# Kernel optimization log

Measured on AMD Instinct MI355X. Metric: run time of the kernel, lower is better.

The kernel has to match this reference:

```python
import jax, jax.numpy as jnp
import numpy as np

IN_F = 1024
OUT_F = 1024

def setup_inputs() -> dict:
    key = jax.random.key(0)
    ks = jax.random.split(key, 7)
    s = 1.0 / np.sqrt(IN_F)
    x = jax.random.normal(ks[0], (4, 2048, IN_F), dtype=jnp.float32)
    Wq = jax.random.uniform(ks[1], (OUT_F, IN_F), jnp.float32, -s, s)
    bq = jax.random.uniform(ks[2], (OUT_F,), jnp.float32, -s, s)
    Wk = jax.random.uniform(ks[3], (OUT_F, IN_F), jnp.float32, -s, s)
    bk = jax.random.uniform(ks[4], (OUT_F,), jnp.float32, -s, s)
    Wv = jax.random.uniform(ks[5], (OUT_F, IN_F), jnp.float32, -s, s)
    bv = jax.random.uniform(ks[6], (OUT_F,), jnp.float32, -s, s)
    return {"x": x, "Wq": Wq, "bq": bq, "Wk": Wk, "bk": bk, "Wv": Wv, "bv": bv}

def reference(x, Wq, bq, Wk, bk, Wv, bv):
    # Projector: ReLU(Linear(x))
    q = jax.nn.relu(jnp.einsum('bsd,od->bso', x, Wq) + bq)  # [B,S,O]
    k = jax.nn.relu(jnp.einsum('bsd,od->bso', x, Wk) + bk)
    v = jax.nn.relu(jnp.einsum('bsd,od->bso', x, Wv) + bv)
    logits = jnp.einsum('bio,bko->bik', q, k)  # unscaled QK^T, [B,S,S]
    scores = jax.nn.softmax(logits, axis=-1)
    out = jnp.einsum('bik,bko->bio', scores, v)
    return out
```

## Files before the change

### kernel.cpp

```cpp
#include <hip/hip_runtime.h>
#include <hip/hip_bf16.h>


#define SEQ 2048
#define DIM 1024
#define NB 4
#define MTOT (NB * SEQ)

typedef __attribute__((ext_vector_type(8))) short frag_ab;
typedef __attribute__((ext_vector_type(4))) float frag_cd;

__device__ __forceinline__ ushort f2bf(float f) {
    union { float f; unsigned u; } x; x.f = f;
    unsigned r = x.u + 0x7fffu + ((x.u >> 16) & 1u);
    return (ushort)(r >> 16);
}

__global__ __launch_bounds__(256) void qkv_kernel(
    const float* __restrict__ x,
    const float* __restrict__ Wq, const float* __restrict__ bq,
    const float* __restrict__ Wk, const float* __restrict__ bk,
    const float* __restrict__ Wv, const float* __restrict__ bv,
    ushort* __restrict__ q, ushort* __restrict__ k, ushort* __restrict__ v)
{
    const float* W; const float* bias; ushort* out;
    if (blockIdx.z == 0)      { W = Wq; bias = bq; out = q; }
    else if (blockIdx.z == 1) { W = Wk; bias = bk; out = k; }
    else                      { W = Wv; bias = bv; out = v; }

    __shared__ ushort As[128][40];
    __shared__ ushort Bs[128][40];

    const int tid  = threadIdx.x;
    const int wave = tid >> 6;
    const int lane = tid & 63;
    const int l16  = lane & 15;
    const int quad = lane >> 4;
    const int m0 = blockIdx.x * 128;
    const int n0 = blockIdx.y * 128;
    const int wm = (wave & 1) * 64;
    const int wn = (wave >> 1) * 64;

    const int sr = tid >> 3;
    const int sc = (tid & 7) * 4;

    frag_cd acc[4][4] = {};

    for (int k0 = 0; k0 < DIM; k0 += 32) {
        #pragma unroll
        for (int i = 0; i < 4; ++i) {
            int row = i * 32 + sr;
            float4 f = *(const float4*)&x[(size_t)(m0 + row) * DIM + k0 + sc];
            ushort4 u; u.x = f2bf(f.x); u.y = f2bf(f.y); u.z = f2bf(f.z); u.w = f2bf(f.w);
            *(ushort4*)&As[row][sc] = u;
        }
        #pragma unroll
        for (int i = 0; i < 4; ++i) {
            int row = i * 32 + sr;
            float4 f = *(const float4*)&W[(size_t)(n0 + row) * DIM + k0 + sc];
            ushort4 u; u.x = f2bf(f.x); u.y = f2bf(f.y); u.z = f2bf(f.z); u.w = f2bf(f.w);
            *(ushort4*)&Bs[row][sc] = u;
        }
        __syncthreads();
        frag_ab af[4], bfr[4];
        #pragma unroll
        for (int mi = 0; mi < 4; ++mi)
            af[mi] = *(const frag_ab*)&As[wm + mi * 16 + l16][quad * 8];
        #pragma unroll
        for (int ni = 0; ni < 4; ++ni)
            bfr[ni] = *(const frag_ab*)&Bs[wn + ni * 16 + l16][quad * 8];
        #pragma unroll
        for (int mi = 0; mi < 4; ++mi)
            #pragma unroll
            for (int ni = 0; ni < 4; ++ni)
                acc[mi][ni] = __builtin_amdgcn_mfma_f32_16x16x32_bf16(
                    af[mi], bfr[ni], acc[mi][ni], 0, 0, 0);
        __syncthreads();
    }

    #pragma unroll
    for (int ni = 0; ni < 4; ++ni) {
        int col = n0 + wn + ni * 16 + l16;
        float bb = bias[col];
        #pragma unroll
        for (int mi = 0; mi < 4; ++mi) {
            int rowb = m0 + wm + mi * 16 + quad * 4;
            #pragma unroll
            for (int r = 0; r < 4; ++r) {
                float val = acc[mi][ni][r] + bb;
                val = val > 0.0f ? val : 0.0f;
                out[(size_t)(rowb + r) * DIM + col] = f2bf(val);
            }
        }
    }
}

__global__ __launch_bounds__(256) void transpose_v(
    const ushort* __restrict__ v, ushort* __restrict__ vt)
{
    __shared__ ushort T[64][72];
    const int bz = blockIdx.z;
    const int s0 = blockIdx.x * 64;
    const int o0 = blockIdx.y * 64;
    const int t  = threadIdx.x;

    #pragma unroll
    for (int p = 0; p < 4; ++p) {
        int sl = p * 16 + (t >> 4);
        int o4 = (t & 15) * 4;
        ushort4 u = *(const ushort4*)&v[(size_t)(bz * SEQ + s0 + sl) * DIM + o0 + o4];
        *(ushort4*)&T[sl][o4] = u;
    }
    __syncthreads();
    #pragma unroll
    for (int p = 0; p < 4; ++p) {
        int ol = p * 16 + (t >> 4);
        int s4 = (t & 15) * 4;
        ushort4 u;
        u.x = T[s4 + 0][ol]; u.y = T[s4 + 1][ol];
        u.z = T[s4 + 2][ol]; u.w = T[s4 + 3][ol];
        *(ushort4*)&vt[(size_t)(bz * DIM + o0 + ol) * SEQ + s0 + s4] = u;
    }
}

__global__ __launch_bounds__(256) void qk_kernel(
    const ushort* __restrict__ q, const ushort* __restrict__ kk,
    float* __restrict__ logits)
{
    __shared__ ushort As[128][40];
    __shared__ ushort Bs[128][40];

    const int tid  = threadIdx.x;
    const int wave = tid >> 6;
    const int lane = tid & 63;
    const int l16  = lane & 15;
    const int quad = lane >> 4;
    const int bz = blockIdx.z;
    const int m0 = blockIdx.x * 128;
    const int n0 = blockIdx.y * 128;
    const int wm = (wave & 1) * 64;
    const int wn = (wave >> 1) * 64;
    const size_t base = (size_t)bz * SEQ;

    const int sr = tid >> 2;
    const int sc = (tid & 3) * 8;

    frag_cd acc[4][4] = {};

    for (int k0 = 0; k0 < DIM; k0 += 32) {
        #pragma unroll
        for (int i = 0; i < 2; ++i) {
            int row = i * 64 + sr;
            *(uint4*)&As[row][sc] =
                *(const uint4*)&q[(base + m0 + row) * DIM + k0 + sc];
            *(uint4*)&Bs[row][sc] =
                *(const uint4*)&kk[(base + n0 + row) * DIM + k0 + sc];
        }
        __syncthreads();
        frag_ab af[4], bfr[4];
        #pragma unroll
        for (int mi = 0; mi < 4; ++mi)
            af[mi] = *(const frag_ab*)&As[wm + mi * 16 + l16][quad * 8];
        #pragma unroll
        for (int ni = 0; ni < 4; ++ni)
            bfr[ni] = *(const frag_ab*)&Bs[wn + ni * 16 + l16][quad * 8];
        #pragma unroll
        for (int mi = 0; mi < 4; ++mi)
            #pragma unroll
            for (int ni = 0; ni < 4; ++ni)
                acc[mi][ni] = __builtin_amdgcn_mfma_f32_16x16x32_bf16(
                    af[mi], bfr[ni], acc[mi][ni], 0, 0, 0);
        __syncthreads();
    }

    #pragma unroll
    for (int mi = 0; mi < 4; ++mi) {
        int rowb = m0 + wm + mi * 16 + quad * 4;
        #pragma unroll
        for (int r = 0; r < 4; ++r) {
            #pragma unroll
            for (int ni = 0; ni < 4; ++ni) {
                int col = n0 + wn + ni * 16 + l16;
                logits[(base + rowb + r) * SEQ + col] = acc[mi][ni][r];
            }
        }
    }
}

__global__ __launch_bounds__(256) void softmax_kernel(float* __restrict__ logits)
{
    float* p = logits + (size_t)blockIdx.x * SEQ;
    const int t = threadIdx.x;
    const int wave = t >> 6, lane = t & 63;

    float4 a = ((const float4*)p)[t];
    float4 b = ((const float4*)p)[t + 256];

    float m = fmaxf(fmaxf(fmaxf(a.x, a.y), fmaxf(a.z, a.w)),
                    fmaxf(fmaxf(b.x, b.y), fmaxf(b.z, b.w)));
    #pragma unroll
    for (int off = 32; off; off >>= 1) m = fmaxf(m, __shfl_down(m, off, 64));

    __shared__ float red[4];
    if (lane == 0) red[wave] = m;
    __syncthreads();
    m = fmaxf(fmaxf(red[0], red[1]), fmaxf(red[2], red[3]));

    a.x = __expf(a.x - m); a.y = __expf(a.y - m);
    a.z = __expf(a.z - m); a.w = __expf(a.w - m);
    b.x = __expf(b.x - m); b.y = __expf(b.y - m);
    b.z = __expf(b.z - m); b.w = __expf(b.w - m);

    float s = (a.x + a.y + a.z + a.w) + (b.x + b.y + b.z + b.w);
    #pragma unroll
    for (int off = 32; off; off >>= 1) s += __shfl_down(s, off, 64);
    __syncthreads();
    if (lane == 0) red[wave] = s;
    __syncthreads();
    s = red[0] + red[1] + red[2] + red[3];
    float inv = 1.0f / s;

    ushort* o = (ushort*)p;
    ushort4 u0, u1;
    u0.x = f2bf(a.x * inv); u0.y = f2bf(a.y * inv);
    u0.z = f2bf(a.z * inv); u0.w = f2bf(a.w * inv);
    u1.x = f2bf(b.x * inv); u1.y = f2bf(b.y * inv);
    u1.z = f2bf(b.z * inv); u1.w = f2bf(b.w * inv);
    ((ushort4*)o)[t]       = u0;
    ((ushort4*)o)[t + 256] = u1;
}

__global__ __launch_bounds__(256) void pv_kernel(
    const ushort* __restrict__ probs, const ushort* __restrict__ vt,
    float* __restrict__ out)
{
    __shared__ ushort As[128][40];
    __shared__ ushort Bs[128][40];

    const int tid  = threadIdx.x;
    const int wave = tid >> 6;
    const int lane = tid & 63;
    const int l16  = lane & 15;
    const int quad = lane >> 4;
    const int bz = blockIdx.z;
    const int m0 = blockIdx.x * 128;
    const int n0 = blockIdx.y * 128;
    const int wm = (wave & 1) * 64;
    const int wn = (wave >> 1) * 64;

    const int sr = tid >> 2;
    const int sc = (tid & 3) * 8;

    frag_cd acc[4][4] = {};

    for (int k0 = 0; k0 < SEQ; k0 += 32) {
        #pragma unroll
        for (int i = 0; i < 2; ++i) {
            int row = i * 64 + sr;
            *(uint4*)&As[row][sc] =
                *(const uint4*)&probs[((size_t)(bz * SEQ + m0 + row)) * 4096 + k0 + sc];
            *(uint4*)&Bs[row][sc] =
                *(const uint4*)&vt[((size_t)(bz * DIM + n0 + row)) * SEQ + k0 + sc];
        }
        __syncthreads();
        frag_ab af[4], bfr[4];
        #pragma unroll
        for (int mi = 0; mi < 4; ++mi)
            af[mi] = *(const frag_ab*)&As[wm + mi * 16 + l16][quad * 8];
        #pragma unroll
        for (int ni = 0; ni < 4; ++ni)
            bfr[ni] = *(const frag_ab*)&Bs[wn + ni * 16 + l16][quad * 8];
        #pragma unroll
        for (int mi = 0; mi < 4; ++mi)
            #pragma unroll
            for (int ni = 0; ni < 4; ++ni)
                acc[mi][ni] = __builtin_amdgcn_mfma_f32_16x16x32_bf16(
                    af[mi], bfr[ni], acc[mi][ni], 0, 0, 0);
        __syncthreads();
    }

    #pragma unroll
    for (int mi = 0; mi < 4; ++mi) {
        int rowb = m0 + wm + mi * 16 + quad * 4;
        #pragma unroll
        for (int r = 0; r < 4; ++r) {
            #pragma unroll
            for (int ni = 0; ni < 4; ++ni) {
                int col = n0 + wn + ni * 16 + l16;
                out[((size_t)(bz * SEQ + rowb + r)) * DIM + col] = acc[mi][ni][r];
            }
        }
    }
}

extern "C" void kernel_launch(void* const* d_in, const int* in_sizes, int n_in,
                              void* d_out, int out_size, void* d_ws, size_t ws_size,
                              hipStream_t stream)
{
    const float* x  = (const float*)d_in[0];
    const float* Wq = (const float*)d_in[1];
    const float* bq = (const float*)d_in[2];
    const float* Wk = (const float*)d_in[3];
    const float* bk = (const float*)d_in[4];
    const float* Wv = (const float*)d_in[5];
    const float* bv = (const float*)d_in[6];
    float* out = (float*)d_out;

    ushort* q  = (ushort*)d_ws;
    ushort* kk = q  + (size_t)MTOT * DIM;
    ushort* v  = kk + (size_t)MTOT * DIM;
    ushort* vt = v  + (size_t)MTOT * DIM;
    float* logits = (float*)(vt + (size_t)MTOT * DIM);

    qkv_kernel<<<dim3(MTOT / 128, DIM / 128, 3), 256, 0, stream>>>(
        x, Wq, bq, Wk, bk, Wv, bv, q, kk, v);
    transpose_v<<<dim3(SEQ / 64, DIM / 64, NB), 256, 0, stream>>>(v, vt);
    qk_kernel<<<dim3(SEQ / 128, SEQ / 128, NB), 256, 0, stream>>>(q, kk, logits);
    softmax_kernel<<<NB * SEQ, 256, 0, stream>>>(logits);
    pv_kernel<<<dim3(SEQ / 128, DIM / 128, NB), 256, 0, stream>>>(
        (const ushort*)logits, vt, out);
}
```

Baseline: 321.9 us.

## Pre-convert inputs to bf16 and load GEMM tiles directly to LDS with swizzle

Adds separate kernels that convert x and the three weight matrices to bf16 once, so the QKV GEMM no longer re-converts fp32 tiles inside its inner loop. All three GEMMs now share a helper that uses global_load_lds to copy 16-byte chunks straight into an unpadded, XOR-swizzled LDS layout, which avoids register staging and bank conflicts. The cost is two extra launches and an extra pass over x through bf16 workspace buffers, with xb aliased over the logits region.

```diff
diff --git a/kernel.cpp b/kernel.cpp
--- a/kernel.cpp
+++ b/kernel.cpp
@@ -16,20 +16,97 @@
     return (ushort)(r >> 16);
 }
 
+typedef __attribute__((address_space(1))) const unsigned int guint;
+typedef __attribute__((address_space(3))) unsigned int luint;
+
+__device__ __forceinline__ void gld_lds16(const void* g, void* l) {
+    __builtin_amdgcn_global_load_lds((guint*)g, (luint*)l, 16, 0, 0);
+}
+
+__device__ __forceinline__ void gemm_tiles(
+    const ushort* __restrict__ A, size_t lda,
+    const ushort* __restrict__ B, size_t ldb, int K,
+    ushort* As, ushort* Bs, frag_cd (&acc)[4][4])
+{
+    const int tid  = threadIdx.x;
+    const int wave = tid >> 6;
+    const int lane = tid & 63;
+    const int l16  = lane & 15;
+    const int quad = lane >> 4;
+    const int sr = wave * 16 + (lane >> 2);
+    const int sc = lane & 3;
+
+    for (int k0 = 0; k0 < K; k0 += 32) {
+        #pragma unroll
+        for (int j = 0; j < 2; ++j) {
+            int row = j * 64 + sr;
+            int cg  = sc ^ ((row >> 1) & 3);
+            ushort* la = As + (j * 64 + wave * 16) * 32;
+            ushort* lb = Bs + (j * 64 + wave * 16) * 32;
+            gld_lds16(A + (size_t)row * lda + k0 + cg * 8, la);
+            gld_lds16(B + (size_t)row * ldb + k0 + cg * 8, lb);
+        }
+        __syncthreads();
+        frag_ab af[4], bfr[4];
+        const int wm = (wave & 1) * 64;
+        const int wn = (wave >> 1) * 64;
+        #pragma unroll
+        for (int mi = 0; mi < 4; ++mi) {
+            int row = wm + mi * 16 + l16;
+            int s = quad ^ ((row >> 1) & 3);
+            af[mi] = *(const frag_ab*)&As[row * 32 + s * 8];
+        }
+        #pragma unroll
+        for (int ni = 0; ni < 4; ++ni) {
+            int row = wn + ni * 16 + l16;
+            int s = quad ^ ((row >> 1) & 3);
+            bfr[ni] = *(const frag_ab*)&Bs[row * 32 + s * 8];
+        }
+        #pragma unroll
+        for (int mi = 0; mi < 4; ++mi)
+            #pragma unroll
+            for (int ni = 0; ni < 4; ++ni)
+                acc[mi][ni] = __builtin_amdgcn_mfma_f32_16x16x32_bf16(
+                    af[mi], bfr[ni], acc[mi][ni], 0, 0, 0);
+        __syncthreads();
+    }
+}
+
+__global__ __launch_bounds__(256) void cvt_x_kernel(
+    const float* __restrict__ src, ushort* __restrict__ dst)
+{
+    size_t i = (size_t)blockIdx.x * 256 + threadIdx.x;
+    float4 f = ((const float4*)src)[i];
+    ushort4 u; u.x = f2bf(f.x); u.y = f2bf(f.y); u.z = f2bf(f.z); u.w = f2bf(f.w);
+    ((ushort4*)dst)[i] = u;
+}
+
+__global__ __launch_bounds__(256) void cvt_w_kernel(
+    const float* __restrict__ Wq, const float* __restrict__ Wk,
+    const float* __restrict__ Wv, ushort* __restrict__ dst)
+{
+    const float* src = blockIdx.y == 0 ? Wq : (blockIdx.y == 1 ? Wk : Wv);
+    ushort* d = dst + (size_t)blockIdx.y * DIM * DIM;
+    size_t i = (size_t)blockIdx.x * 256 + threadIdx.x;
+    float4 f = ((const float4*)src)[i];
+    ushort4 u; u.x = f2bf(f.x); u.y = f2bf(f.y); u.z = f2bf(f.z); u.w = f2bf(f.w);
+    ((ushort4*)d)[i] = u;
+}
+
 __global__ __launch_bounds__(256) void qkv_kernel(
-    const float* __restrict__ x,
-    const float* __restrict__ Wq, const float* __restrict__ bq,
-    const float* __restrict__ Wk, const float* __restrict__ bk,
-    const float* __restrict__ Wv, const float* __restrict__ bv,
+    const ushort* __restrict__ xb, const ushort* __restrict__ Wb,
+    const float* __restrict__ bq, const float* __restrict__ bk,
+    const float* __restrict__ bv,
     ushort* __restrict__ q, ushort* __restrict__ k, ushort* __restrict__ v)
 {
-    const float* W; const float* bias; ushort* out;
-    if (blockIdx.z == 0)      { W = Wq; bias = bq; out = q; }
-    else if (blockIdx.z == 1) { W = Wk; bias = bk; out = k; }
-    else                      { W = Wv; bias = bv; out = v; }
-
-    __shared__ ushort As[128][40];
-    __shared__ ushort Bs[128][40];
+    const float* bias; ushort* out;
+    if (blockIdx.z == 0)      { bias = bq; out = q; }
+    else if (blockIdx.z == 1) { bias = bk; out = k; }
+    else                      { bias = bv; out = v; }
+    const ushort* W = Wb + (size_t)blockIdx.z * DIM * DIM;
+
+    __shared__ ushort As[128 * 32];
+    __shared__ ushort Bs[128 * 32];
 
     const int tid  = threadIdx.x;
     const int wave = tid >> 6;
@@ -41,42 +118,9 @@
     const int wm = (wave & 1) * 64;
     const int wn = (wave >> 1) * 64;
 
-    const int sr = tid >> 3;
-    const int sc = (tid & 7) * 4;
-
     frag_cd acc[4][4] = {};
-
-    for (int k0 = 0; k0 < DIM; k0 += 32) {
-        #pragma unroll
-        for (int i = 0; i < 4; ++i) {
-            int row = i * 32 + sr;
-            float4 f = *(const float4*)&x[(size_t)(m0 + row) * DIM + k0 + sc];
-            ushort4 u; u.x = f2bf(f.x); u.y = f2bf(f.y); u.z = f2bf(f.z); u.w = f2bf(f.w);
-            *(ushort4*)&As[row][sc] = u;
-        }
-        #pragma unroll
-        for (int i = 0; i < 4; ++i) {
-            int row = i * 32 + sr;
-            float4 f = *(const float4*)&W[(size_t)(n0 + row) * DIM + k0 + sc];
-            ushort4 u; u.x = f2bf(f.x); u.y = f2bf(f.y); u.z = f2bf(f.z); u.w = f2bf(f.w);
-            *(ushort4*)&Bs[row][sc] = u;
-        }
-        __syncthreads();
-        frag_ab af[4], bfr[4];
-        #pragma unroll
-        for (int mi = 0; mi < 4; ++mi)
-            af[mi] = *(const frag_ab*)&As[wm + mi * 16 + l16][quad * 8];
-        #pragma unroll
-        for (int ni = 0; ni < 4; ++ni)
-            bfr[ni] = *(const frag_ab*)&Bs[wn + ni * 16 + l16][quad * 8];
-        #pragma unroll
-        for (int mi = 0; mi < 4; ++mi)
-            #pragma unroll
-            for (int ni = 0; ni < 4; ++ni)
-                acc[mi][ni] = __builtin_amdgcn_mfma_f32_16x16x32_bf16(
-                    af[mi], bfr[ni], acc[mi][ni], 0, 0, 0);
-        __syncthreads();
-    }
+    gemm_tiles(xb + (size_t)m0 * DIM, DIM, W + (size_t)n0 * DIM, DIM, DIM,
+               As, Bs, acc);
 
     #pragma unroll
     for (int ni = 0; ni < 4; ++ni) {
@@ -127,8 +171,8 @@
     const ushort* __restrict__ q, const ushort* __restrict__ kk,
     float* __restrict__ logits)
 {
-    __shared__ ushort As[128][40];
-    __shared__ ushort Bs[128][40];
+    __shared__ ushort As[128 * 32];
+    __shared__ ushort Bs[128 * 32];
 
     const int tid  = threadIdx.x;
     const int wave = tid >> 6;
@@ -142,48 +186,20 @@
     const int wn = (wave >> 1) * 64;
     const size_t base = (size_t)bz * SEQ;
 
-    const int sr = tid >> 2;
-    const int sc = (tid & 3) * 8;
-
     frag_cd acc[4][4] = {};
-
-    for (int k0 = 0; k0 < DIM; k0 += 32) {
-        #pragma unroll
-        for (int i = 0; i < 2; ++i) {
-            int row = i * 64 + sr;
-            *(uint4*)&As[row][sc] =
-                *(const uint4*)&q[(base + m0 + row) * DIM + k0 + sc];
-            *(uint4*)&Bs[row][sc] =
-                *(const uint4*)&kk[(base + n0 + row) * DIM + k0 + sc];
-        }
-        __syncthreads();
-        frag_ab af[4], bfr[4];
-        #pragma unroll
-        for (int mi = 0; mi < 4; ++mi)
-            af[mi] = *(const frag_ab*)&As[wm + mi * 16 + l16][quad * 8];
-        #pragma unroll
-        for (int ni = 0; ni < 4; ++ni)
-            bfr[ni] = *(const frag_ab*)&Bs[wn + ni * 16 + l16][quad * 8];
-        #pragma unroll
-        for (int mi = 0; mi < 4; ++mi)
-            #pragma unroll
-            for (int ni = 0; ni < 4; ++ni)
-                acc[mi][ni] = __builtin_amdgcn_mfma_f32_16x16x32_bf16(
-                    af[mi], bfr[ni], acc[mi][ni], 0, 0, 0);
-        __syncthreads();
-    }
+    gemm_tiles(q + (base + m0) * DIM, DIM, kk + (base + n0) * DIM, DIM, DIM,
+               As, Bs, acc);
 
     #pragma unroll
     for (int mi = 0; mi < 4; ++mi) {
         int rowb = m0 + wm + mi * 16 + quad * 4;
         #pragma unroll
-        for (int r = 0; r < 4; ++r) {
+        for (int r = 0; r < 4; ++r)
             #pragma unroll
             for (int ni = 0; ni < 4; ++ni) {
                 int col = n0 + wn + ni * 16 + l16;
                 logits[(base + rowb + r) * SEQ + col] = acc[mi][ni][r];
             }
-        }
     }
 }
 
@@ -234,8 +250,8 @@
     const ushort* __restrict__ probs, const ushort* __restrict__ vt,
     float* __restrict__ out)
 {
-    __shared__ ushort As[128][40];
-    __shared__ ushort Bs[128][40];
+    __shared__ ushort As[128 * 32];
+    __shared__ ushort Bs[128 * 32];
 
     const int tid  = threadIdx.x;
     const int wave = tid >> 6;
@@ -248,48 +264,21 @@
     const int wm = (wave & 1) * 64;
     const int wn = (wave >> 1) * 64;
 
-    const int sr = tid >> 2;
-    const int sc = (tid & 3) * 8;
-
     frag_cd acc[4][4] = {};
-
-    for (int k0 = 0; k0 < SEQ; k0 += 32) {
-        #pragma unroll
-        for (int i = 0; i < 2; ++i) {
-            int row = i * 64 + sr;
-            *(uint4*)&As[row][sc] =
-                *(const uint4*)&probs[((size_t)(bz * SEQ + m0 + row)) * 4096 + k0 + sc];
-            *(uint4*)&Bs[row][sc] =
-                *(const uint4*)&vt[((size_t)(bz * DIM + n0 + row)) * SEQ + k0 + sc];
-        }
-        __syncthreads();
-        frag_ab af[4], bfr[4];
-        #pragma unroll
-        for (int mi = 0; mi < 4; ++mi)
-            af[mi] = *(const frag_ab*)&As[wm + mi * 16 + l16][quad * 8];
-        #pragma unroll
-        for (int ni = 0; ni < 4; ++ni)
-            bfr[ni] = *(const frag_ab*)&Bs[wn + ni * 16 + l16][quad * 8];
-        #pragma unroll
-        for (int mi = 0; mi < 4; ++mi)
-            #pragma unroll
-            for (int ni = 0; ni < 4; ++ni)
-                acc[mi][ni] = __builtin_amdgcn_mfma_f32_16x16x32_bf16(
-                    af[mi], bfr[ni], acc[mi][ni], 0, 0, 0);
-        __syncthreads();
-    }
+    gemm_tiles(probs + ((size_t)(bz * SEQ + m0)) * 4096, 4096,
+               vt + ((size_t)(bz * DIM + n0)) * SEQ, SEQ, SEQ,
+               As, Bs, acc);
 
     #pragma unroll
     for (int mi = 0; mi < 4; ++mi) {
         int rowb = m0 + wm + mi * 16 + quad * 4;
         #pragma unroll
-        for (int r = 0; r < 4; ++r) {
+        for (int r = 0; r < 4; ++r)
             #pragma unroll
             for (int ni = 0; ni < 4; ++ni) {
                 int col = n0 + wn + ni * 16 + l16;
                 out[((size_t)(bz * SEQ + rowb + r)) * DIM + col] = acc[mi][ni][r];
             }
-        }
     }
 }
 
@@ -306,14 +295,20 @@
     const float* bv = (const float*)d_in[6];
     float* out = (float*)d_out;
 
-    ushort* q  = (ushort*)d_ws;
-    ushort* kk = q  + (size_t)MTOT * DIM;
-    ushort* v  = kk + (size_t)MTOT * DIM;
-    ushort* vt = v  + (size_t)MTOT * DIM;
-    float* logits = (float*)(vt + (size_t)MTOT * DIM);
+    char* ws = (char*)d_ws;
+    ushort* q      = (ushort*)(ws);
+    ushort* kk     = (ushort*)(ws + ((size_t)16 << 20));
+    ushort* v      = (ushort*)(ws + ((size_t)32 << 20));
+    ushort* vt     = (ushort*)(ws + ((size_t)48 << 20));
+    float*  logits = (float*) (ws + ((size_t)64 << 20));
+    ushort* xb     = (ushort*)(ws + ((size_t)64 << 20));
+    ushort* Wb     = (ushort*)(ws + ((size_t)80 << 20));
+
+    cvt_x_kernel<<<dim3(MTOT * DIM / 4 / 256), 256, 0, stream>>>(x, xb);
+    cvt_w_kernel<<<dim3(DIM * DIM / 4 / 256, 3), 256, 0, stream>>>(Wq, Wk, Wv, Wb);
 
     qkv_kernel<<<dim3(MTOT / 128, DIM / 128, 3), 256, 0, stream>>>(
-        x, Wq, bq, Wk, bk, Wv, bv, q, kk, v);
+        xb, Wb, bq, bk, bv, q, kk, v);
     transpose_v<<<dim3(SEQ / 64, DIM / 64, NB), 256, 0, stream>>>(v, vt);
     qk_kernel<<<dim3(SEQ / 128, SEQ / 128, NB), 256, 0, stream>>>(q, kk, logits);
     softmax_kernel<<<NB * SEQ, 256, 0, stream>>>(logits);
```

Result: faster. 286.0 us (-11.2%).
